# Kernel optimization log

Measured on AMD Instinct MI355X. Metric: run time of the kernel, lower is better.

The kernel has to match this reference:

```python
import jax, jax.numpy as jnp
import numpy as np

B, H, W, MD = 1, 128, 256, 66
LD, NH, HD, S = 64, 8, 8, 16   # learnable_dim, n_heads, head_dim, shared_hidden
KS, J = 21, 25                 # disco basis functions, neighbors per output point
HMLP, FFN_H = 32, 256

def _gelu(x):
    return jax.nn.gelu(x, approximate=False)

def _build_nbr():
    # 5x5 geodesic window: clamp at poles (lat), wrap in longitude
    ii = np.clip(np.arange(H)[:, None] + np.arange(-2, 3)[None, :], 0, H - 1)  # [H,5]
    jj = (np.arange(W)[:, None] + np.arange(-2, 3)[None, :]) % W               # [W,5]
    nbr = ii[:, None, :, None] * W + jj[None, :, None, :]                      # [H,W,5,5]
    return nbr.reshape(H * W, J).astype(np.int32)

def setup_inputs() -> dict:
    key = jax.random.key(0)
    ks = jax.random.split(key, 16)
    x = jax.random.normal(ks[0], (B, H, W, MD), dtype=jnp.float32)
    nbr = jnp.asarray(_build_nbr())
    # sparse DiSCO basis values (nonnegative, piecewise-linear style), weights, bias
    psi = jax.random.uniform(ks[1], (H * W, J, KS), dtype=jnp.float32) / J
    disco_w = jax.random.normal(ks[2], (S, KS), dtype=jnp.float32) * 0.2
    disco_b = jax.random.normal(ks[3], (S,), dtype=jnp.float32) * 0.02
    # LatModulator: 2 -> 2S -> 2S MLP on (sin_lat, cos_lat)
    lm_w1 = jax.random.normal(ks[4], (2, 2 * S), dtype=jnp.float32) * 0.3
    lm_b1 = jnp.zeros((2 * S,), dtype=jnp.float32)
    lm_w2 = jax.random.normal(ks[5], (2 * S, 2 * S), dtype=jnp.float32) * 0.2
    lm_b2 = jnp.concatenate([jnp.ones((S,), jnp.float32), jnp.zeros((S,), jnp.float32)])  # gamma~1, beta~0
    # per-head MLPs: S -> HMLP -> 1, stacked over heads
    h_w1 = jax.random.normal(ks[6], (NH, S, HMLP), dtype=jnp.float32) * (1.0 / np.sqrt(S))
    h_b1 = jnp.zeros((NH, HMLP), dtype=jnp.float32)
    h_w2 = jax.random.normal(ks[7], (NH, HMLP), dtype=jnp.float32) * (1.0 / np.sqrt(HMLP))
    h_b2 = jnp.zeros((NH,), dtype=jnp.float32)
    # FFN: model_dim -> FFN_H -> learnable_dim; last-2 input cols zeroed (init per source)
    f_w1 = jax.random.normal(ks[8], (MD, FFN_H), dtype=jnp.float32) * (1.0 / np.sqrt(MD))
    f_w1 = f_w1.at[-2:, :].set(0.0)
    f_b1 = jnp.zeros((FFN_H,), dtype=jnp.float32)
    f_w2 = jax.random.normal(ks[9], (FFN_H, LD), dtype=jnp.float32) * (1.0 / np.sqrt(FFN_H))
    f_b2 = jnp.zeros((LD,), dtype=jnp.float32)
    return dict(x=x, nbr=nbr, psi=psi, disco_w=disco_w, disco_b=disco_b,
                lm_w1=lm_w1, lm_b1=lm_b1, lm_w2=lm_w2, lm_b2=lm_b2,
                h_w1=h_w1, h_b1=h_b1, h_w2=h_w2, h_b2=h_b2,
                f_w1=f_w1, f_b1=f_b1, f_w2=f_w2, f_b2=f_b2)

def reference(x, nbr, psi, disco_w, disco_b, lm_w1, lm_b1, lm_w2, lm_b2,
              h_w1, h_b1, h_w2, h_b2, f_w1, f_b1, f_w2, f_b2):
    x_learn = x[..., :LD]               # (B,H,W,LD)
    sin_cos = x[..., LD:]               # (B,H,W,2)
    # --- sparse DiSCO conv, 1 input channel per map, shared over all maps ---
    xmaps = x_learn.transpose(0, 3, 1, 2).reshape(B * LD, H * W)   # (BL, P)
    xg = xmaps[:, nbr]                                             # (BL, P, J) irregular gather
    Wp = jnp.einsum('pjk,ok->pjo', psi, disco_w)                   # (P, J, S)
    y = jnp.einsum('npj,pjo->npo', xg, Wp) + disco_b               # (BL, P, S)
    disco_out = y.reshape(B, LD, H, W, S).transpose(0, 2, 3, 1, 4) # (B,H,W,LD,S)
    # --- FiLM latitude modulation ---
    scr = sin_cos[:, :, 0, :]                                      # (B,H,2)
    m = _gelu(scr @ lm_w1 + lm_b1) @ lm_w2 + lm_b2                 # (B,H,2S)
    gamma = m[..., :S][:, :, None, None, :]                        # (B,H,1,1,S)
    beta = m[..., S:][:, :, None, None, :]
    disco_out = disco_out * gamma + beta
    # --- per-head MLPs (S -> HMLP -> 1), vectorized over heads ---
    d5 = disco_out.reshape(B, H, W, NH, HD, S)
    h1 = _gelu(jnp.einsum('bhwnds,nsc->bhwndc', d5, h_w1) + h_b1[:, None, :].reshape(NH, 1, HMLP))
    ho = jnp.einsum('bhwndc,nc->bhwnd', h1, h_w2) + h_b2[None, None, None, :, None]
    x_learn2 = ho.reshape(B, H, W, LD) + x_learn                   # residual
    # --- FFN channel mixing ---
    x_full = jnp.concatenate([x_learn2, sin_cos], axis=-1)
    f = _gelu(x_full @ f_w1 + f_b1) @ f_w2 + f_b2                  # (B,H,W,LD)
    out_learn = f + x_learn2
    return jnp.concatenate([out_learn, sin_cos], axis=-1)
```

## Files before the change

### kernel.cpp

```cpp
#include <hip/hip_runtime.h>
#include <math.h>

#define HDIM 128
#define WDIM 256
#define NPIX (HDIM*WDIM)
#define LD 64
#define S 16
#define J 25
#define KS 21
#define NH 8
#define HMLP 32
#define FFN_H 256
#define PSI_ROW (J*KS)
#define WP_ROW (J*S)

__device__ __forceinline__ float gelu_exact(float v) {
    return 0.5f * v * (1.0f + erff(v * 0.70710678118654752440f));
}

__device__ __forceinline__ float gelu_fast(float x) {
    float x2 = x * x;
    float a  = __builtin_fmaf(x2, 0.035677408136f, 0.7978845608028654f);
    float z  = a * x * 2.885390081777927f;
    z = fmaxf(-30.f, fminf(30.f, z));
    float e  = __builtin_exp2f(z);
    float th = (e - 1.f) * __builtin_amdgcn_rcpf(e + 1.f);
    float s  = 0.5f * x;
    return __builtin_fmaf(s, th, s);
}

__global__ __launch_bounds__(128) void k_mod(
    const float* __restrict__ x, const float* __restrict__ lm_w1,
    const float* __restrict__ lm_b1, const float* __restrict__ lm_w2,
    const float* __restrict__ lm_b2, float* __restrict__ gb)
{
    int h = threadIdx.x;
    float s0 = x[h * WDIM * 66 + 64];
    float s1 = x[h * WDIM * 66 + 65];
    float t[32];
#pragma unroll
    for (int j = 0; j < 32; ++j)
        t[j] = gelu_exact(s0 * lm_w1[j] + s1 * lm_w1[32 + j] + lm_b1[j]);
#pragma unroll
    for (int j = 0; j < 32; ++j) {
        float m = lm_b2[j];
#pragma unroll
        for (int cc = 0; cc < 32; ++cc) m += t[cc] * lm_w2[cc * 32 + j];
        gb[h * 32 + j] = m;
    }
}

__global__ __launch_bounds__(256) void k_wp(
    const float* __restrict__ psi, const float* __restrict__ disco_w,
    float* __restrict__ wp)
{
    __shared__ alignas(16) float psi_s[4][J * 24];
    __shared__ alignas(16) float dw_s[16 * 28];

    const int tid = threadIdx.x;
    const int wid = tid >> 6;
    const int lane = tid & 63;

    for (int i = tid; i < 16 * KS; i += 256) dw_s[(i / KS) * 28 + (i % KS)] = disco_w[i];
    __syncthreads();

    const int p = blockIdx.x * 4 + wid;
    const float* pr = psi + (size_t)p * PSI_ROW;
#pragma unroll
    for (int t = 0; t < 9; ++t) {
        int idx = t * 64 + lane;
        if (idx < PSI_ROW) {
            int j = idx / KS, k = idx - j * KS;
            psi_s[wid][j * 24 + k] = pr[idx];
        }
    }
    asm volatile("s_waitcnt lgkmcnt(0) vmcnt(0)" ::: "memory");

#pragma unroll
    for (int i = 0; i < 7; ++i) {
        int e = i * 64 + lane;
        if (e < WP_ROW) {
            int j = e >> 4, o = e & 15;
            const float* pj = &psi_s[wid][j * 24];
            const float* wo = &dw_s[o * 28];
            float acc = pj[20] * wo[20];
#pragma unroll
            for (int t = 0; t < 5; ++t) {
                float4 a = *(const float4*)(pj + t * 4);
                float4 b = *(const float4*)(wo + t * 4);
                acc += a.x * b.x + a.y * b.y + a.z * b.z + a.w * b.w;
            }
            wp[(size_t)p * WP_ROW + e] = acc;
        }
    }
}

__device__ __forceinline__ float head_mlp(
    const float y[16], int n, const float* __restrict__ hw1_s,
    const float* __restrict__ hb1_s, const float* __restrict__ hw2_s)
{
    float ho = 0.f;
#pragma unroll
    for (int c8 = 0; c8 < 4; ++c8) {
        float t8[8];
        {
            const float4* hb = (const float4*)&hb1_s[n * 36 + c8 * 8];
            float4 b0 = hb[0], b1 = hb[1];
            t8[0] = b0.x; t8[1] = b0.y; t8[2] = b0.z; t8[3] = b0.w;
            t8[4] = b1.x; t8[5] = b1.y; t8[6] = b1.z; t8[7] = b1.w;
        }
#pragma unroll
        for (int s = 0; s < 16; ++s) {
            float ys = y[s];
            const float* hr = &hw1_s[n * 516 + s * 32 + c8 * 8];
            float4 h0 = *(const float4*)(hr);
            float4 h1 = *(const float4*)(hr + 4);
            t8[0] += ys * h0.x; t8[1] += ys * h0.y;
            t8[2] += ys * h0.z; t8[3] += ys * h0.w;
            t8[4] += ys * h1.x; t8[5] += ys * h1.y;
            t8[6] += ys * h1.z; t8[7] += ys * h1.w;
        }
#pragma unroll
        for (int j = 0; j < 8; ++j)
            ho += gelu_fast(t8[j]) * hw2_s[n * 33 + c8 * 8 + j];
    }
    return ho;
}

__global__ __launch_bounds__(256) void k_disco(
    const float* __restrict__ x, const float* __restrict__ wp,
    const float* __restrict__ disco_b, const float* __restrict__ gb,
    const float* __restrict__ h_w1, const float* __restrict__ h_b1,
    const float* __restrict__ h_w2, const float* __restrict__ h_b2,
    float* __restrict__ x2out)
{
    __shared__ alignas(16) float4 wp_s[4][J * 4];
    __shared__ alignas(16) float hw1_s[8 * 516];
    __shared__ alignas(16) float hb1_s[8 * 36];
    __shared__ float hw2_s[8 * 33];
    __shared__ alignas(16) float db_s[16];
    __shared__ float hb2_s[8];

    const int tid = threadIdx.x;
    const int wid = tid >> 6;
    const int lane = tid & 63;

    for (int i = tid; i < NH * S * HMLP; i += 256) {
        int n = i >> 9;
        hw1_s[n * 516 + (i & 511)] = h_w1[i];
    }
    { int i = tid; hw2_s[(i >> 5) * 33 + (i & 31)] = h_w2[i]; }
    { int i = tid; hb1_s[(i >> 5) * 36 + (i & 31)] = h_b1[i]; }
    if (tid < 16) db_s[tid] = disco_b[tid];
    if (tid < 8)  hb2_s[tid] = h_b2[tid];
    __syncthreads();

    const int pbase = (blockIdx.x * 4 + wid) * 8;
    const int h = pbase >> 8;
    const int w0 = pbase & 255;
    const int c = lane;
    const int n = lane >> 3;

    int rowoff[5];
#pragma unroll
    for (int a = 0; a < 5; ++a) {
        int hh = h + a - 2;
        hh = hh < 0 ? 0 : (hh > HDIM - 1 ? HDIM - 1 : hh);
        rowoff[a] = hh << 8;
    }
    const float* gbp = gb + h * 32;

    for (int it = 0; it < 8; ++it) {
        const int p = pbase + it;
        const int w = w0 + it;

        const float4* wpg = (const float4*)(wp + (size_t)p * WP_ROW);
#pragma unroll
        for (int t = 0; t < 2; ++t) {
            int idx = t * 64 + lane;
            if (idx < J * 4) wp_s[wid][idx] = wpg[idx];
        }
        asm volatile("s_waitcnt lgkmcnt(0) vmcnt(0)" ::: "memory");

        float y[16];
#pragma unroll
        for (int o4 = 0; o4 < 4; ++o4) {
            float4 d = ((const float4*)db_s)[o4];
            y[o4 * 4 + 0] = d.x; y[o4 * 4 + 1] = d.y;
            y[o4 * 4 + 2] = d.z; y[o4 * 4 + 3] = d.w;
        }

        float xc = 0.f;
#pragma unroll
        for (int a = 0; a < 5; ++a) {
#pragma unroll
            for (int b = 0; b < 5; ++b) {
                int ww = (w + b - 2) & 255;
                float xv = x[(size_t)(rowoff[a] + ww) * 66 + c];
                if (a == 2 && b == 2) xc = xv;
                const float4* wrow = &wp_s[wid][(a * 5 + b) * 4];
#pragma unroll
                for (int o4 = 0; o4 < 4; ++o4) {
                    float4 wv = wrow[o4];
                    y[o4 * 4 + 0] += xv * wv.x;
                    y[o4 * 4 + 1] += xv * wv.y;
                    y[o4 * 4 + 2] += xv * wv.z;
                    y[o4 * 4 + 3] += xv * wv.w;
                }
            }
        }

#pragma unroll
        for (int o = 0; o < 16; ++o)
            y[o] = y[o] * gbp[o] + gbp[16 + o];

        float ho = head_mlp(y, n, hw1_s, hb1_s, hw2_s);

        x2out[(size_t)p * 64 + c] = ho + hb2_s[n] + xc;
    }
}

__global__ __launch_bounds__(64) void k_ffn1(
    const float* __restrict__ x2, const float* __restrict__ f_w1,
    const float* __restrict__ f_b1, float* __restrict__ f1t)
{
    __shared__ float x2s[64 * 67];
    const int tid = threadIdx.x;
    const int qc = blockIdx.x & 3;
    const int p0 = (blockIdx.x >> 2) * 64;

    for (int i = 0; i < 64; ++i)
        x2s[i * 67 + tid] = x2[(size_t)(p0 + i) * 64 + tid];
    __syncthreads();

    const int p = p0 + tid;
    float acc[64];
#pragma unroll
    for (int c4 = 0; c4 < 16; ++c4) {
        float4 bv = *(const float4*)(f_b1 + qc * 64 + c4 * 4);
        acc[c4 * 4 + 0] = bv.x; acc[c4 * 4 + 1] = bv.y;
        acc[c4 * 4 + 2] = bv.z; acc[c4 * 4 + 3] = bv.w;
    }

    for (int k = 0; k < 64; ++k) {
        float xv = x2s[tid * 67 + k];
        const float4* wr = (const float4*)(f_w1 + k * FFN_H + qc * 64);
#pragma unroll
        for (int c4 = 0; c4 < 16; ++c4) {
            float4 wv = wr[c4];
            acc[c4 * 4 + 0] += xv * wv.x;
            acc[c4 * 4 + 1] += xv * wv.y;
            acc[c4 * 4 + 2] += xv * wv.z;
            acc[c4 * 4 + 3] += xv * wv.w;
        }
    }
#pragma unroll
    for (int cc = 0; cc < 64; ++cc)
        f1t[(size_t)(qc * 64 + cc) * NPIX + p] = gelu_fast(acc[cc]);
}

__global__ __launch_bounds__(64) void k_ffn2(
    const float* __restrict__ x, const float* __restrict__ x2,
    const float* __restrict__ f1t, const float* __restrict__ f_w2,
    const float* __restrict__ f_b2, float* __restrict__ out)
{
    const int tid = threadIdx.x;
    const int half = blockIdx.x & 1;
    const int p0 = (blockIdx.x >> 1) * 64;
    const int p = p0 + tid;
    const int cbase = half * 32;

    float acc[32];
#pragma unroll
    for (int c4 = 0; c4 < 8; ++c4) {
        float4 bv = *(const float4*)(f_b2 + cbase + c4 * 4);
        acc[c4 * 4 + 0] = bv.x; acc[c4 * 4 + 1] = bv.y;
        acc[c4 * 4 + 2] = bv.z; acc[c4 * 4 + 3] = bv.w;
    }

    for (int q = 0; q < FFN_H; ++q) {
        float f1v = f1t[(size_t)q * NPIX + p];
        const float4* wr = (const float4*)(f_w2 + q * 64 + cbase);
#pragma unroll
        for (int c4 = 0; c4 < 8; ++c4) {
            float4 wv = wr[c4];
            acc[c4 * 4 + 0] += f1v * wv.x;
            acc[c4 * 4 + 1] += f1v * wv.y;
            acc[c4 * 4 + 2] += f1v * wv.z;
            acc[c4 * 4 + 3] += f1v * wv.w;
        }
    }

    const float4* x2p = (const float4*)(x2 + (size_t)p * 64 + cbase);
#pragma unroll
    for (int c4 = 0; c4 < 8; ++c4) {
        float4 xv = x2p[c4];
        out[(size_t)p * 66 + cbase + c4 * 4 + 0] = acc[c4 * 4 + 0] + xv.x;
        out[(size_t)p * 66 + cbase + c4 * 4 + 1] = acc[c4 * 4 + 1] + xv.y;
        out[(size_t)p * 66 + cbase + c4 * 4 + 2] = acc[c4 * 4 + 2] + xv.z;
        out[(size_t)p * 66 + cbase + c4 * 4 + 3] = acc[c4 * 4 + 3] + xv.w;
    }
    if (half) {
        out[(size_t)p * 66 + 64] = x[(size_t)p * 66 + 64];
        out[(size_t)p * 66 + 65] = x[(size_t)p * 66 + 65];
    }
}

extern "C" void kernel_launch(void* const* d_in, const int* in_sizes, int n_in,
                              void* d_out, int out_size, void* d_ws, size_t ws_size,
                              hipStream_t stream) {
    const float* x       = (const float*)d_in[0];
    const float* psi     = (const float*)d_in[2];
    const float* disco_w = (const float*)d_in[3];
    const float* disco_b = (const float*)d_in[4];
    const float* lm_w1   = (const float*)d_in[5];
    const float* lm_b1   = (const float*)d_in[6];
    const float* lm_w2   = (const float*)d_in[7];
    const float* lm_b2   = (const float*)d_in[8];
    const float* h_w1    = (const float*)d_in[9];
    const float* h_b1    = (const float*)d_in[10];
    const float* h_w2    = (const float*)d_in[11];
    const float* h_b2    = (const float*)d_in[12];
    const float* f_w1    = (const float*)d_in[13];
    const float* f_b1    = (const float*)d_in[14];
    const float* f_w2    = (const float*)d_in[15];
    const float* f_b2    = (const float*)d_in[16];
    float* out = (float*)d_out;

    float* gb  = (float*)d_ws;
    float* x2  = gb + 4096;
    float* wp  = x2 + (size_t)NPIX * 64;
    float* f1t = wp;

    k_mod  <<<1,    128, 0, stream>>>(x, lm_w1, lm_b1, lm_w2, lm_b2, gb);
    k_wp   <<<8192, 256, 0, stream>>>(psi, disco_w, wp);
    k_disco<<<1024, 256, 0, stream>>>(x, wp, disco_b, gb,
                                      h_w1, h_b1, h_w2, h_b2, x2);
    k_ffn1 <<<2048, 64,  0, stream>>>(x2, f_w1, f_b1, f1t);
    k_ffn2 <<<1024, 64,  0, stream>>>(x, x2, f1t, f_w2, f_b2, out);
}
```

Before: 389.9 us.

## Restructure FFN kernels with register-resident weights and LDS-staged tiles

k_ffn1 now keeps each thread's column of f_w1 in registers and streams pixel rows through LDS, transposing results through an LDS tile before writing f1t. k_ffn2 stages its half of f_w2 into LDS and uses 256-thread blocks instead of reading weights from global memory per iteration. k_disco hoists the FiLM gamma/beta, disco bias and head bias into registers. The aim is to cut repeated global weight reads and small-block launch overhead. The costs are higher register pressure (64-float weight array), large LDS use, and far fewer blocks (512 and 256), which may leave the GPU underoccupied.

```diff
diff --git a/kernel.cpp b/kernel.cpp
--- a/kernel.cpp
+++ b/kernel.cpp
@@ -138,7 +138,6 @@
     __shared__ alignas(16) float hw1_s[8 * 516];
     __shared__ alignas(16) float hb1_s[8 * 36];
     __shared__ float hw2_s[8 * 33];
-    __shared__ alignas(16) float db_s[16];
     __shared__ float hb2_s[8];
 
     const int tid = threadIdx.x;
@@ -151,7 +150,6 @@
     }
     { int i = tid; hw2_s[(i >> 5) * 33 + (i & 31)] = h_w2[i]; }
     { int i = tid; hb1_s[(i >> 5) * 36 + (i & 31)] = h_b1[i]; }
-    if (tid < 16) db_s[tid] = disco_b[tid];
     if (tid < 8)  hb2_s[tid] = h_b2[tid];
     __syncthreads();
 
@@ -168,7 +166,21 @@
         hh = hh < 0 ? 0 : (hh > HDIM - 1 ? HDIM - 1 : hh);
         rowoff[a] = hh << 8;
     }
-    const float* gbp = gb + h * 32;
+
+    float gbr[16], ber[16], dbr[16];
+    {
+        const float* gbp = gb + h * 32;
+#pragma unroll
+        for (int o4 = 0; o4 < 4; ++o4) {
+            float4 g  = *(const float4*)(gbp + o4 * 4);
+            float4 be = *(const float4*)(gbp + 16 + o4 * 4);
+            float4 d  = *(const float4*)(disco_b + o4 * 4);
+            gbr[o4*4+0] = g.x;  gbr[o4*4+1] = g.y;  gbr[o4*4+2] = g.z;  gbr[o4*4+3] = g.w;
+            ber[o4*4+0] = be.x; ber[o4*4+1] = be.y; ber[o4*4+2] = be.z; ber[o4*4+3] = be.w;
+            dbr[o4*4+0] = d.x;  dbr[o4*4+1] = d.y;  dbr[o4*4+2] = d.z;  dbr[o4*4+3] = d.w;
+        }
+    }
+    const float hb2r = hb2_s[n];
 
     for (int it = 0; it < 8; ++it) {
         const int p = pbase + it;
@@ -184,11 +196,7 @@
 
         float y[16];
 #pragma unroll
-        for (int o4 = 0; o4 < 4; ++o4) {
-            float4 d = ((const float4*)db_s)[o4];
-            y[o4 * 4 + 0] = d.x; y[o4 * 4 + 1] = d.y;
-            y[o4 * 4 + 2] = d.z; y[o4 * 4 + 3] = d.w;
-        }
+        for (int o = 0; o < 16; ++o) y[o] = dbr[o];
 
         float xc = 0.f;
 #pragma unroll
@@ -212,63 +220,71 @@
 
 #pragma unroll
         for (int o = 0; o < 16; ++o)
-            y[o] = y[o] * gbp[o] + gbp[16 + o];
+            y[o] = y[o] * gbr[o] + ber[o];
 
         float ho = head_mlp(y, n, hw1_s, hb1_s, hw2_s);
 
-        x2out[(size_t)p * 64 + c] = ho + hb2_s[n] + xc;
-    }
-}
-
-__global__ __launch_bounds__(64) void k_ffn1(
+        x2out[(size_t)p * 64 + c] = ho + hb2r + xc;
+    }
+}
+
+__global__ __launch_bounds__(256) void k_ffn1(
     const float* __restrict__ x2, const float* __restrict__ f_w1,
     const float* __restrict__ f_b1, float* __restrict__ f1t)
 {
-    __shared__ float x2s[64 * 67];
+    __shared__ alignas(16) float rowbuf[4][64];
+    __shared__ float ttile[4][64][65];
+
     const int tid = threadIdx.x;
-    const int qc = blockIdx.x & 3;
-    const int p0 = (blockIdx.x >> 2) * 64;
-
-    for (int i = 0; i < 64; ++i)
-        x2s[i * 67 + tid] = x2[(size_t)(p0 + i) * 64 + tid];
-    __syncthreads();
-
-    const int p = p0 + tid;
-    float acc[64];
-#pragma unroll
-    for (int c4 = 0; c4 < 16; ++c4) {
-        float4 bv = *(const float4*)(f_b1 + qc * 64 + c4 * 4);
-        acc[c4 * 4 + 0] = bv.x; acc[c4 * 4 + 1] = bv.y;
-        acc[c4 * 4 + 2] = bv.z; acc[c4 * 4 + 3] = bv.w;
-    }
-
-    for (int k = 0; k < 64; ++k) {
-        float xv = x2s[tid * 67 + k];
-        const float4* wr = (const float4*)(f_w1 + k * FFN_H + qc * 64);
-#pragma unroll
-        for (int c4 = 0; c4 < 16; ++c4) {
-            float4 wv = wr[c4];
-            acc[c4 * 4 + 0] += xv * wv.x;
-            acc[c4 * 4 + 1] += xv * wv.y;
-            acc[c4 * 4 + 2] += xv * wv.z;
-            acc[c4 * 4 + 3] += xv * wv.w;
-        }
-    }
-#pragma unroll
-    for (int cc = 0; cc < 64; ++cc)
-        f1t[(size_t)(qc * 64 + cc) * NPIX + p] = gelu_fast(acc[cc]);
-}
-
-__global__ __launch_bounds__(64) void k_ffn2(
+    const int w   = tid >> 6;
+    const int ln  = tid & 63;
+    const int p0  = blockIdx.x * 64;
+
+    float wreg[64];
+#pragma unroll
+    for (int k = 0; k < 64; ++k)
+        wreg[k] = f_w1[k * FFN_H + w * 64 + ln];
+    const float bias = f_b1[w * 64 + ln];
+
+    for (int px = 0; px < 64; ++px) {
+        const int p = p0 + px;
+        rowbuf[w][ln] = x2[(size_t)p * 64 + ln];
+        asm volatile("s_waitcnt lgkmcnt(0) vmcnt(0)" ::: "memory");
+
+        float acc = bias;
+#pragma unroll
+        for (int k4 = 0; k4 < 16; ++k4) {
+            float4 xv = *(const float4*)&rowbuf[w][k4 * 4];
+            acc += xv.x * wreg[k4 * 4 + 0] + xv.y * wreg[k4 * 4 + 1]
+                 + xv.z * wreg[k4 * 4 + 2] + xv.w * wreg[k4 * 4 + 3];
+        }
+        ttile[w][px][ln] = gelu_fast(acc);
+    }
+    asm volatile("s_waitcnt lgkmcnt(0)" ::: "memory");
+
+    for (int r = 0; r < 64; ++r)
+        f1t[(size_t)(w * 64 + r) * NPIX + p0 + ln] = ttile[w][ln][r];
+}
+
+__global__ __launch_bounds__(256) void k_ffn2(
     const float* __restrict__ x, const float* __restrict__ x2,
     const float* __restrict__ f1t, const float* __restrict__ f_w2,
     const float* __restrict__ f_b2, float* __restrict__ out)
 {
+    __shared__ alignas(16) float w2s[256 * 32];
+
     const int tid = threadIdx.x;
-    const int half = blockIdx.x & 1;
-    const int p0 = (blockIdx.x >> 1) * 64;
-    const int p = p0 + tid;
+    const int wv  = tid >> 6;
+    const int ln  = tid & 63;
+    const int half  = blockIdx.x & 1;
     const int cbase = half * 32;
+    const int p0    = (blockIdx.x >> 1) * 256;
+
+    for (int i = tid; i < 256 * 32; i += 256)
+        w2s[i] = f_w2[(i >> 5) * 64 + cbase + (i & 31)];
+    __syncthreads();
+
+    const int p = p0 + wv * 64 + ln;
 
     float acc[32];
 #pragma unroll
@@ -280,7 +296,7 @@
 
     for (int q = 0; q < FFN_H; ++q) {
         float f1v = f1t[(size_t)q * NPIX + p];
-        const float4* wr = (const float4*)(f_w2 + q * 64 + cbase);
+        const float4* wr = (const float4*)&w2s[q * 32];
 #pragma unroll
         for (int c4 = 0; c4 < 8; ++c4) {
             float4 wv = wr[c4];
@@ -336,6 +352,6 @@
     k_wp   <<<8192, 256, 0, stream>>>(psi, disco_w, wp);
     k_disco<<<1024, 256, 0, stream>>>(x, wp, disco_b, gb,
                                       h_w1, h_b1, h_w2, h_b2, x2);
-    k_ffn1 <<<2048, 64,  0, stream>>>(x2, f_w1, f_b1, f1t);
-    k_ffn2 <<<1024, 64,  0, stream>>>(x, x2, f1t, f_w2, f_b2, out);
-}
+    k_ffn1 <<<512,  256, 0, stream>>>(x2, f_w1, f_b1, f1t);
+    k_ffn2 <<<256,  256, 0, stream>>>(x, x2, f1t, f_w2, f_b2, out);
+}
```

Measured after the change: 440.3 us. 1.13x slower.
